# Performance work log

Hardware: AMD Instinct MI355X
Metric: run time of the kernel (lower is better)

Reference implementation:

```python
import jax, jax.numpy as jnp
import numpy as np

N = 60000      # nodes in batch (max_num_cg_nodes_in_batch = 80000)
E = 150000     # edges per edge type
T = 4          # primary edge types (doubled by add_backwards_edges -> 8)
D = 64         # hidden / embedding size
V = 10000      # subtoken vocab
S = 5          # max subtokens per node label
TIMESTEPS = [7, 1]


def setup_inputs() -> dict:
    key = jax.random.key(0)
    ks = jax.random.split(key, 12)
    sc = 1.0 / np.sqrt(D)
    return {
        "node_subtokens": jax.random.randint(ks[0], (N, S), 0, V),
        "adjacency_lists": jax.random.randint(ks[1], (T, E, 2), 0, N),
        "embed_table": jax.random.normal(ks[2], (V, D), jnp.float32) * 0.1,
        "proj_W": jax.random.normal(ks[3], (D, D), jnp.float32) * sc,
        "edge_W0": jax.random.normal(ks[4], (2 * T, D, D), jnp.float32) * sc,
        "edge_W1": jax.random.normal(ks[5], (2 * T, D, D), jnp.float32) * sc,
        "gru0_Wx": jax.random.normal(ks[6], (D, 3 * D), jnp.float32) * sc,
        "gru0_Wh": jax.random.normal(ks[7], (D, 3 * D), jnp.float32) * sc,
        "gru0_b": jnp.zeros((3 * D,), jnp.float32),
        "gru1_Wx": jax.random.normal(ks[8], (2 * D, 3 * D), jnp.float32) * sc,
        "gru1_Wh": jax.random.normal(ks[9], (D, 3 * D), jnp.float32) * sc,
        "gru1_b": jnp.zeros((3 * D,), jnp.float32),
    }


def _gru(x, h, Wx, Wh, b):
    gx = x @ Wx + b          # [N, 3D]
    gh = h @ Wh              # [N, 3D]
    xr, xu, xc = jnp.split(gx, 3, axis=-1)
    hr, hu, hc = jnp.split(gh, 3, axis=-1)
    r = jax.nn.sigmoid(xr + hr)
    u = jax.nn.sigmoid(xu + hu)
    c = jnp.tanh(xc + r * hc)
    return u * h + (1.0 - u) * c


def reference(node_subtokens, adjacency_lists, embed_table, proj_W,
              edge_W0, edge_W1, gru0_Wx, gru0_Wh, gru0_b,
              gru1_Wx, gru1_Wh, gru1_b):
    # Effective edge types: forward + backward (add_backwards_edges=True)
    srcs = jnp.concatenate([adjacency_lists[:, :, 0], adjacency_lists[:, :, 1]], 0)  # [2T, E]
    dsts = jnp.concatenate([adjacency_lists[:, :, 1], adjacency_lists[:, :, 0]], 0)  # [2T, E]
    flat_dsts = dsts.reshape(-1)

    def aggregate(h, edge_W):
        gathered = h[srcs]                                 # [2T, E, D] gather
        msgs = jnp.einsum('ted,tdk->tek', gathered, edge_W)  # per-edge-type transform
        m = jax.ops.segment_max(msgs.reshape(-1, D), flat_dsts, num_segments=N)
        # nodes with no incoming edges get -inf from segment_max -> zero them
        return jnp.where(jnp.isfinite(m), m, 0.0)

    # Subtoken embedding: mean-pool subtoken embeddings, project to hidden
    node_emb = embed_table[node_subtokens].mean(axis=1)    # [N, D]
    h_init = node_emb @ proj_W                             # [N, D]

    # Layer 0: 7 timesteps, no residual
    h = h_init
    for _ in range(TIMESTEPS[0]):
        h = _gru(aggregate(h, edge_W0), h, gru0_Wx, gru0_Wh, gru0_b)

    # Layer 1: 1 timestep, residual from layer index 0 (= initial node states)
    for _ in range(TIMESTEPS[1]):
        msg = aggregate(h, edge_W1)
        h = _gru(jnp.concatenate([h_init, msg], axis=-1), h, gru1_Wx, gru1_Wh, gru1_b)

    return h  # [N, D] final node representations
```

## Files before the change

kernel.cpp:

```cpp
#include <hip/hip_runtime.h>

typedef short v8s __attribute__((ext_vector_type(8)));
typedef float v4f __attribute__((ext_vector_type(4)));

__device__ __forceinline__ unsigned short f2bf(float x) {
  unsigned u = __float_as_uint(x);
  u = u + 0x7FFFu + ((u >> 16) & 1u);
  return (unsigned short)(u >> 16);
}
__device__ __forceinline__ float bf2f(unsigned short b) {
  return __uint_as_float(((unsigned)b) << 16);
}
__device__ __forceinline__ float sigmoidf_(float x) {
  return 1.f / (1.f + __expf(-x));
}
__device__ __forceinline__ float tanhf_(float x) {
  x = fminf(fmaxf(x, -20.f), 20.f);
  float e2 = __expf(2.f * x);
  return (e2 - 1.f) / (e2 + 1.f);
}
__device__ __forceinline__ int swz(int row, int byteInRow) {
  return row * 128 + (byteInRow ^ ((row & 7) << 4));
}

__device__ __forceinline__ void wprep_one(const float* W, unsigned short* O,
                                          int K, int J, int idx) {
  int nkc = K >> 5, nct = J >> 4;
  int j = idx & 7, lane = (idx >> 3) & 63;
  int rest = idx >> 9;
  int ct = rest % nct; rest /= nct;
  int kc = rest % nkc; rest /= nkc;
  int p = rest & 1, t = rest >> 1;
  int row = kc * 32 + (lane >> 4) * 8 + j;
  int col = ct * 16 + (lane & 15);
  float v = W[(size_t)t * K * J + (size_t)row * J + col];
  unsigned short hi = f2bf(v);
  O[idx] = p ? f2bf(v - bf2f(hi)) : hi;
}

__global__ void k_wprep_all(
    const float* eW0, const float* eW1, const float* projW,
    const float* g0Wx, const float* g0Wh, const float* g1Wx, const float* g1Wh,
    unsigned short* eW0f, unsigned short* eW1f, unsigned short* projf,
    unsigned short* g0xf, unsigned short* g0hf,
    unsigned short* g1xf, unsigned short* g1hf) {
  int rel = blockIdx.x * 256 + threadIdx.x;
  if (rel < 65536) { wprep_one(eW0, eW0f, 64, 64, rel); return; }
  rel -= 65536;
  if (rel < 65536) { wprep_one(eW1, eW1f, 64, 64, rel); return; }
  rel -= 65536;
  if (rel < 8192)  { wprep_one(projW, projf, 64, 64, rel); return; }
  rel -= 8192;
  if (rel < 24576) { wprep_one(g0Wx, g0xf, 64, 192, rel); return; }
  rel -= 24576;
  if (rel < 24576) { wprep_one(g0Wh, g0hf, 64, 192, rel); return; }
  rel -= 24576;
  if (rel < 49152) { wprep_one(g1Wx, g1xf, 128, 192, rel); return; }
  rel -= 49152;
  if (rel < 24576) { wprep_one(g1Wh, g1hf, 64, 192, rel); return; }
}

__global__ __launch_bounds__(256) void k_embed(
    const int* __restrict__ toks, const float* __restrict__ embed,
    unsigned short* __restrict__ eh, unsigned short* __restrict__ el, int N) {
  int w = threadIdx.x >> 6, lane = threadIdx.x & 63;
  int n = blockIdx.x * 4 + w;
  if (n >= N) return;
  float acc = 0.f;
#pragma unroll
  for (int s = 0; s < 5; ++s)
    acc += embed[(size_t)toks[n * 5 + s] * 64 + lane];
  float v = acc * 0.2f;
  unsigned short h = f2bf(v);
  eh[(size_t)n * 64 + lane] = h;
  el[(size_t)n * 64 + lane] = f2bf(v - bf2f(h));
}

__global__ void k_counts(const int* __restrict__ adj, int* __restrict__ counts, int E) {
  int e = blockIdx.x * 256 + threadIdx.x;
  if (e >= E) return;
  int t4 = blockIdx.y;
  int2 ab = *(const int2*)&adj[(size_t)(t4 * E + e) * 2];
  atomicAdd(&counts[ab.y], 1);
  atomicAdd(&counts[ab.x], 1);
}

__global__ __launch_bounds__(1024) void k_scan(const int* __restrict__ counts,
                                               int* __restrict__ offsets,
                                               int* __restrict__ cursor, int n) {
  __shared__ int part[1024];
  int tid = threadIdx.x;
  int chunk = (((n + 1023) >> 10) + 3) & ~3;
  int begin = tid * chunk;
  int end = min(begin + chunk, n);
  int s = 0;
  int i = begin;
  for (; i + 4 <= end; i += 4) {
    int4 v = *(const int4*)&counts[i];
    s += v.x + v.y + v.z + v.w;
  }
  for (; i < end; ++i) s += counts[i];
  part[tid] = s;
  __syncthreads();
  for (int off = 1; off < 1024; off <<= 1) {
    int v = (tid >= off) ? part[tid - off] : 0;
    __syncthreads();
    part[tid] += v;
    __syncthreads();
  }
  int run = part[tid] - s;
  i = begin;
  for (; i + 4 <= end; i += 4) {
    int4 c = *(const int4*)&counts[i];
    int4 o;
    o.x = run; o.y = run + c.x; o.z = o.y + c.y; o.w = o.z + c.z;
    *(int4*)&offsets[i] = o;
    *(int4*)&cursor[i] = o;
    run = o.w + c.w;
  }
  for (; i < end; ++i) {
    offsets[i] = run; cursor[i] = run; run += counts[i];
  }
  if (tid == 1023) offsets[n] = part[1023];
}

__global__ void k_fill(const int* __restrict__ adj, int* __restrict__ cursor,
                       int* __restrict__ entries, int E, int N) {
  int e = blockIdx.x * 256 + threadIdx.x;
  if (e >= E) return;
  int t4 = blockIdx.y;
  int2 ab = *(const int2*)&adj[(size_t)(t4 * E + e) * 2];
  int p1 = atomicAdd(&cursor[ab.y], 1);
  entries[p1] = t4 * N + ab.x;
  int p2 = atomicAdd(&cursor[ab.x], 1);
  entries[p2] = (t4 + 4) * N + ab.y;
}

__global__ __launch_bounds__(256) void k_proj(
    const unsigned short* __restrict__ A0h, const unsigned short* __restrict__ A0l,
    const unsigned short* __restrict__ Wf,
    unsigned short* __restrict__ h_hi, unsigned short* __restrict__ h_lo,
    unsigned short* __restrict__ hinit_b, int N) {
  int tid = threadIdx.x;
  int wv = tid >> 6, lane = tid & 63;
  int lr = lane & 15, lg = lane >> 4;
  int m0 = blockIdx.x * 128 + wv * 32;
  v4f acc[2][4] = {};
#pragma unroll
  for (int kc = 0; kc < 2; ++kc) {
    v8s ah[2], al[2];
#pragma unroll
    for (int mt = 0; mt < 2; ++mt) {
      int row = min(m0 + mt * 16 + lr, N - 1);
      size_t off = (size_t)row * 64 + kc * 32 + lg * 8;
      ah[mt] = *(const v8s*)&A0h[off];
      al[mt] = *(const v8s*)&A0l[off];
    }
#pragma unroll
    for (int ct = 0; ct < 4; ++ct) {
      v8s bh = *(const v8s*)&Wf[((size_t)(kc * 4 + ct)) * 512 + lane * 8];
      v8s bl = *(const v8s*)&Wf[((size_t)((2 + kc) * 4 + ct)) * 512 + lane * 8];
#pragma unroll
      for (int mt = 0; mt < 2; ++mt) {
        acc[mt][ct] = __builtin_amdgcn_mfma_f32_16x16x32_bf16(ah[mt], bh, acc[mt][ct], 0, 0, 0);
        acc[mt][ct] = __builtin_amdgcn_mfma_f32_16x16x32_bf16(al[mt], bh, acc[mt][ct], 0, 0, 0);
        acc[mt][ct] = __builtin_amdgcn_mfma_f32_16x16x32_bf16(ah[mt], bl, acc[mt][ct], 0, 0, 0);
      }
    }
  }
#pragma unroll
  for (int ct = 0; ct < 4; ++ct)
#pragma unroll
    for (int mt = 0; mt < 2; ++mt)
#pragma unroll
      for (int r = 0; r < 4; ++r) {
        int m = m0 + mt * 16 + lg * 4 + r;
        if (m >= N) continue;
        int col = ct * 16 + lr;
        float v = acc[mt][ct][r];
        unsigned short hb = f2bf(v);
        h_hi[(size_t)m * 64 + col] = hb;
        h_lo[(size_t)m * 64 + col] = f2bf(v - bf2f(hb));
        hinit_b[(size_t)m * 64 + col] = hb;
      }
}

__global__ __launch_bounds__(256) void k_mm_t(
    const unsigned short* __restrict__ A0h, const unsigned short* __restrict__ A0l,
    const unsigned short* __restrict__ Wf, unsigned short* __restrict__ C16,
    int N) {
  int tid = threadIdx.x;
  int wv = tid >> 6, lane = tid & 63;
  int lr = lane & 15, lg = lane >> 4;
  int y = blockIdx.y;
  const unsigned short* W0 = Wf + (size_t)y * 8192;
  const unsigned short* W1 = Wf + (size_t)(y + 4) * 8192;
  unsigned short* C0 = C16 + (size_t)y * N * 64;
  unsigned short* C1 = C16 + (size_t)(y + 4) * N * 64;
  int m0 = blockIdx.x * 128 + wv * 32;
  v4f acc0[2][4] = {}, acc1[2][4] = {};
#pragma unroll
  for (int kc = 0; kc < 2; ++kc) {
    v8s ah[2], al[2];
#pragma unroll
    for (int mt = 0; mt < 2; ++mt) {
      int row = min(m0 + mt * 16 + lr, N - 1);
      size_t off = (size_t)row * 64 + kc * 32 + lg * 8;
      ah[mt] = *(const v8s*)&A0h[off];
      al[mt] = *(const v8s*)&A0l[off];
    }
#pragma unroll
    for (int ct = 0; ct < 4; ++ct) {
      v8s bh0 = *(const v8s*)&W0[((size_t)(kc * 4 + ct)) * 512 + lane * 8];
      v8s bl0 = *(const v8s*)&W0[((size_t)((2 + kc) * 4 + ct)) * 512 + lane * 8];
      v8s bh1 = *(const v8s*)&W1[((size_t)(kc * 4 + ct)) * 512 + lane * 8];
      v8s bl1 = *(const v8s*)&W1[((size_t)((2 + kc) * 4 + ct)) * 512 + lane * 8];
#pragma unroll
      for (int mt = 0; mt < 2; ++mt) {
        acc0[mt][ct] = __builtin_amdgcn_mfma_f32_16x16x32_bf16(ah[mt], bh0, acc0[mt][ct], 0, 0, 0);
        acc0[mt][ct] = __builtin_amdgcn_mfma_f32_16x16x32_bf16(al[mt], bh0, acc0[mt][ct], 0, 0, 0);
        acc0[mt][ct] = __builtin_amdgcn_mfma_f32_16x16x32_bf16(ah[mt], bl0, acc0[mt][ct], 0, 0, 0);
        acc1[mt][ct] = __builtin_amdgcn_mfma_f32_16x16x32_bf16(ah[mt], bh1, acc1[mt][ct], 0, 0, 0);
        acc1[mt][ct] = __builtin_amdgcn_mfma_f32_16x16x32_bf16(al[mt], bh1, acc1[mt][ct], 0, 0, 0);
        acc1[mt][ct] = __builtin_amdgcn_mfma_f32_16x16x32_bf16(ah[mt], bl1, acc1[mt][ct], 0, 0, 0);
      }
    }
  }
#pragma unroll
  for (int ct = 0; ct < 4; ++ct)
#pragma unroll
    for (int mt = 0; mt < 2; ++mt)
#pragma unroll
      for (int r = 0; r < 4; ++r) {
        int m = m0 + mt * 16 + lg * 4 + r;
        if (m < N) {
          C0[(size_t)m * 64 + ct * 16 + lr] = f2bf(acc0[mt][ct][r]);
          C1[(size_t)m * 64 + ct * 16 + lr] = f2bf(acc1[mt][ct][r]);
        }
      }
}

__global__ __launch_bounds__(256) void k_aggmax(
    const unsigned short* __restrict__ Htb, const int* __restrict__ offsets,
    const int* __restrict__ entries, unsigned short* __restrict__ mh, int N) {
  int w = threadIdx.x >> 6, lane = threadIdx.x & 63;
  int n = blockIdx.x * 4 + w;
  if (n >= N) return;
  int beg = offsets[n], end = offsets[n + 1];
  int g = lane >> 4, q = lane & 15;
  float a0 = -3.4e38f, a1 = a0, a2 = a0, a3 = a0;
  float b0 = a0, b1 = a0, b2 = a0, b3 = a0;
  float c0 = a0, c1 = a0, c2 = a0, c3 = a0;
  float d0 = a0, d1 = a0, d2 = a0, d3 = a0;
  int i = beg;
  for (; i + 16 <= end; i += 16) {
    int eA = entries[i + g];
    int eB = entries[i + 4 + g];
    int eC = entries[i + 8 + g];
    int eD = entries[i + 12 + g];
    ushort4 va = *(const ushort4*)&Htb[(size_t)eA * 64 + q * 4];
    ushort4 vb = *(const ushort4*)&Htb[(size_t)eB * 64 + q * 4];
    ushort4 vc = *(const ushort4*)&Htb[(size_t)eC * 64 + q * 4];
    ushort4 vd = *(const ushort4*)&Htb[(size_t)eD * 64 + q * 4];
    a0 = fmaxf(a0, bf2f(va.x)); a1 = fmaxf(a1, bf2f(va.y));
    a2 = fmaxf(a2, bf2f(va.z)); a3 = fmaxf(a3, bf2f(va.w));
    b0 = fmaxf(b0, bf2f(vb.x)); b1 = fmaxf(b1, bf2f(vb.y));
    b2 = fmaxf(b2, bf2f(vb.z)); b3 = fmaxf(b3, bf2f(vb.w));
    c0 = fmaxf(c0, bf2f(vc.x)); c1 = fmaxf(c1, bf2f(vc.y));
    c2 = fmaxf(c2, bf2f(vc.z)); c3 = fmaxf(c3, bf2f(vc.w));
    d0 = fmaxf(d0, bf2f(vd.x)); d1 = fmaxf(d1, bf2f(vd.y));
    d2 = fmaxf(d2, bf2f(vd.z)); d3 = fmaxf(d3, bf2f(vd.w));
  }
  for (; i + 8 <= end; i += 8) {
    int eA = entries[i + g];
    int eB = entries[i + 4 + g];
    ushort4 va = *(const ushort4*)&Htb[(size_t)eA * 64 + q * 4];
    ushort4 vb = *(const ushort4*)&Htb[(size_t)eB * 64 + q * 4];
    a0 = fmaxf(a0, bf2f(va.x)); a1 = fmaxf(a1, bf2f(va.y));
    a2 = fmaxf(a2, bf2f(va.z)); a3 = fmaxf(a3, bf2f(va.w));
    b0 = fmaxf(b0, bf2f(vb.x)); b1 = fmaxf(b1, bf2f(vb.y));
    b2 = fmaxf(b2, bf2f(vb.z)); b3 = fmaxf(b3, bf2f(vb.w));
  }
  for (; i < end; i += 4) {
    int idx = min(i + g, end - 1);
    int e = entries[idx];
    ushort4 va = *(const ushort4*)&Htb[(size_t)e * 64 + q * 4];
    a0 = fmaxf(a0, bf2f(va.x)); a1 = fmaxf(a1, bf2f(va.y));
    a2 = fmaxf(a2, bf2f(va.z)); a3 = fmaxf(a3, bf2f(va.w));
  }
  a0 = fmaxf(fmaxf(a0, b0), fmaxf(c0, d0));
  a1 = fmaxf(fmaxf(a1, b1), fmaxf(c1, d1));
  a2 = fmaxf(fmaxf(a2, b2), fmaxf(c2, d2));
  a3 = fmaxf(fmaxf(a3, b3), fmaxf(c3, d3));
  a0 = fmaxf(a0, __shfl_xor(a0, 16)); a1 = fmaxf(a1, __shfl_xor(a1, 16));
  a2 = fmaxf(a2, __shfl_xor(a2, 16)); a3 = fmaxf(a3, __shfl_xor(a3, 16));
  a0 = fmaxf(a0, __shfl_xor(a0, 32)); a1 = fmaxf(a1, __shfl_xor(a1, 32));
  a2 = fmaxf(a2, __shfl_xor(a2, 32)); a3 = fmaxf(a3, __shfl_xor(a3, 32));
  if (g == 0) {
    ushort4 o;
    if (end > beg) {
      o.x = f2bf(a0); o.y = f2bf(a1); o.z = f2bf(a2); o.w = f2bf(a3);
    } else {
      o.x = 0; o.y = 0; o.z = 0; o.w = 0;
    }
    *(ushort4*)&mh[(size_t)n * 64 + q * 4] = o;
  }
}

template <int FINAL>
__global__ __launch_bounds__(256) void k_gt(
    const unsigned short* __restrict__ x0, const unsigned short* __restrict__ x1,
    unsigned short* __restrict__ hh, unsigned short* __restrict__ hl,
    const unsigned short* __restrict__ Wxf, const unsigned short* __restrict__ Whf,
    const float* __restrict__ bias, const unsigned short* __restrict__ eWf,
    unsigned short* __restrict__ HtW, float* __restrict__ outF, int N) {
  __shared__ __align__(16) char lds_hs[FINAL ? 16 : 128 * 128];
  int tid = threadIdx.x;
  int wv = tid >> 6, lane = tid & 63;
  int lr = lane & 15, lg = lane >> 4;
  int lbase = wv * 32;
  int m0 = blockIdx.x * 128 + lbase;

  const int NKCX = FINAL ? 4 : 2;
  v4f acc[2][12] = {};
  v4f acch[2][4] = {};
#pragma unroll
  for (int kc = 0; kc < NKCX; ++kc) {
    const unsigned short* X = (FINAL && kc >= 2) ? x1 : x0;
    int kcl = kc & 1;
    v8s ax[2];
#pragma unroll
    for (int mt = 0; mt < 2; ++mt) {
      int row = min(m0 + mt * 16 + lr, N - 1);
      ax[mt] = *(const v8s*)&X[(size_t)row * 64 + kcl * 32 + lg * 8];
    }
#pragma unroll
    for (int ct = 0; ct < 12; ++ct) {
      v8s bh = *(const v8s*)&Wxf[((size_t)(kc * 12 + ct)) * 512 + lane * 8];
      v8s bl = *(const v8s*)&Wxf[((size_t)((NKCX + kc) * 12 + ct)) * 512 + lane * 8];
#pragma unroll
      for (int mt = 0; mt < 2; ++mt) {
        acc[mt][ct] = __builtin_amdgcn_mfma_f32_16x16x32_bf16(ax[mt], bh, acc[mt][ct], 0, 0, 0);
        acc[mt][ct] = __builtin_amdgcn_mfma_f32_16x16x32_bf16(ax[mt], bl, acc[mt][ct], 0, 0, 0);
      }
    }
  }
#pragma unroll
  for (int kc = 0; kc < 2; ++kc) {
    v8s ah[2], al[2];
#pragma unroll
    for (int mt = 0; mt < 2; ++mt) {
      int row = min(m0 + mt * 16 + lr, N - 1);
      size_t off = (size_t)row * 64 + kc * 32 + lg * 8;
      ah[mt] = *(const v8s*)&hh[off];
      al[mt] = *(const v8s*)&hl[off];
    }
#pragma unroll
    for (int ct = 0; ct < 12; ++ct) {
      v8s bh = *(const v8s*)&Whf[((size_t)(kc * 12 + ct)) * 512 + lane * 8];
      v8s bl = *(const v8s*)&Whf[((size_t)((2 + kc) * 12 + ct)) * 512 + lane * 8];
#pragma unroll
      for (int mt = 0; mt < 2; ++mt) {
        v4f* d = (ct < 8) ? &acc[mt][ct] : &acch[mt][ct - 8];
        *d = __builtin_amdgcn_mfma_f32_16x16x32_bf16(ah[mt], bh, *d, 0, 0, 0);
        *d = __builtin_amdgcn_mfma_f32_16x16x32_bf16(al[mt], bh, *d, 0, 0, 0);
        *d = __builtin_amdgcn_mfma_f32_16x16x32_bf16(ah[mt], bl, *d, 0, 0, 0);
      }
    }
  }
#pragma unroll
  for (int mt = 0; mt < 2; ++mt)
#pragma unroll
    for (int ctg = 0; ctg < 4; ++ctg)
#pragma unroll
      for (int r = 0; r < 4; ++r) {
        int m = m0 + mt * 16 + lg * 4 + r;
        int col = ctg * 16 + lr;
        unsigned short hbv = hh[(size_t)min(m, N - 1) * 64 + col];
        unsigned short hlv = hl[(size_t)min(m, N - 1) * 64 + col];
        float hv = bf2f(hbv) + bf2f(hlv);
        float rr = sigmoidf_(acc[mt][ctg][r] + bias[col]);
        float uu = sigmoidf_(acc[mt][ctg + 4][r] + bias[64 + col]);
        float cc = tanhf_(acc[mt][ctg + 8][r] + bias[128 + col] + rr * acch[mt][ctg][r]);
        float ho = uu * hv + (1.f - uu) * cc;
        if (FINAL) {
          if (m < N) outF[(size_t)m * 64 + col] = ho;
        } else {
          unsigned short ohi = f2bf(ho);
          unsigned short olo = f2bf(ho - bf2f(ohi));
          if (m < N) {
            hh[(size_t)m * 64 + col] = ohi;
            hl[(size_t)m * 64 + col] = olo;
          }
          int row = lbase + mt * 16 + lg * 4 + r;
          *(unsigned short*)(lds_hs + swz(row, col * 2)) = ohi;
        }
      }

  if (FINAL) return;

  v8s tah[2][2];
#pragma unroll
  for (int kc = 0; kc < 2; ++kc)
#pragma unroll
    for (int mt = 0; mt < 2; ++mt) {
      int row = lbase + mt * 16 + lr;
      tah[kc][mt] = *(const v8s*)(lds_hs + swz(row, kc * 64 + lg * 16));
    }
#pragma unroll
  for (int y = 0; y < 4; ++y) {
    const unsigned short* W0 = eWf + (size_t)y * 8192;
    const unsigned short* W1 = eWf + (size_t)(y + 4) * 8192;
    unsigned short* C0 = HtW + (size_t)y * N * 64;
    unsigned short* C1 = HtW + (size_t)(y + 4) * N * 64;
    v4f acc0[2][4] = {}, acc1[2][4] = {};
#pragma unroll
    for (int kc = 0; kc < 2; ++kc)
#pragma unroll
      for (int ct = 0; ct < 4; ++ct) {
        v8s bh0 = *(const v8s*)&W0[((size_t)(kc * 4 + ct)) * 512 + lane * 8];
        v8s bl0 = *(const v8s*)&W0[((size_t)((2 + kc) * 4 + ct)) * 512 + lane * 8];
        v8s bh1 = *(const v8s*)&W1[((size_t)(kc * 4 + ct)) * 512 + lane * 8];
        v8s bl1 = *(const v8s*)&W1[((size_t)((2 + kc) * 4 + ct)) * 512 + lane * 8];
#pragma unroll
        for (int mt = 0; mt < 2; ++mt) {
          acc0[mt][ct] = __builtin_amdgcn_mfma_f32_16x16x32_bf16(tah[kc][mt], bh0, acc0[mt][ct], 0, 0, 0);
          acc0[mt][ct] = __builtin_amdgcn_mfma_f32_16x16x32_bf16(tah[kc][mt], bl0, acc0[mt][ct], 0, 0, 0);
          acc1[mt][ct] = __builtin_amdgcn_mfma_f32_16x16x32_bf16(tah[kc][mt], bh1, acc1[mt][ct], 0, 0, 0);
          acc1[mt][ct] = __builtin_amdgcn_mfma_f32_16x16x32_bf16(tah[kc][mt], bl1, acc1[mt][ct], 0, 0, 0);
        }
      }
#pragma unroll
    for (int ct = 0; ct < 4; ++ct)
#pragma unroll
      for (int mt = 0; mt < 2; ++mt)
#pragma unroll
        for (int r = 0; r < 4; ++r) {
          int m = m0 + mt * 16 + lg * 4 + r;
          if (m < N) {
            C0[(size_t)m * 64 + ct * 16 + lr] = f2bf(acc0[mt][ct][r]);
            C1[(size_t)m * 64 + ct * 16 + lr] = f2bf(acc1[mt][ct][r]);
          }
        }
  }
}

extern "C" void kernel_launch(void* const* d_in, const int* in_sizes, int n_in,
                              void* d_out, int out_size, void* d_ws, size_t ws_size,
                              hipStream_t stream) {
  const int*   toks  = (const int*)d_in[0];
  const int*   adj   = (const int*)d_in[1];
  const float* embed = (const float*)d_in[2];
  const float* projW = (const float*)d_in[3];
  const float* eW0   = (const float*)d_in[4];
  const float* eW1   = (const float*)d_in[5];
  const float* g0Wx  = (const float*)d_in[6];
  const float* g0Wh  = (const float*)d_in[7];
  const float* g0b   = (const float*)d_in[8];
  const float* g1Wx  = (const float*)d_in[9];
  const float* g1Wh  = (const float*)d_in[10];
  const float* g1b   = (const float*)d_in[11];
  float* out = (float*)d_out;

  int N = in_sizes[0] / 5;
  int E = in_sizes[1] / 8;
  size_t ND = (size_t)N * 64;

  char* p = (char*)d_ws;
  unsigned short* Htb     = (unsigned short*)p; p += 8 * ND * 2;
  unsigned short* h_hi    = (unsigned short*)p; p += ND * 2;
  unsigned short* h_lo    = (unsigned short*)p; p += ND * 2;
  unsigned short* hinit_b = (unsigned short*)p; p += ND * 2;
  unsigned short* m_hi    = (unsigned short*)p; p += ND * 2;
  int* offsets = (int*)p; p += (size_t)(N + 64) * sizeof(int);
  int* cnt_cur = (int*)p; p += (size_t)(N + 64) * sizeof(int);
  int* entries = (int*)p; p += (size_t)8 * E * sizeof(int);
  unsigned short* eW0f  = (unsigned short*)p; p += 65536 * 2;
  unsigned short* eW1f  = (unsigned short*)p; p += 65536 * 2;
  unsigned short* projf = (unsigned short*)p; p += 8192 * 2;
  unsigned short* g0xf  = (unsigned short*)p; p += 24576 * 2;
  unsigned short* g0hf  = (unsigned short*)p; p += 24576 * 2;
  unsigned short* g1xf  = (unsigned short*)p; p += 49152 * 2;
  unsigned short* g1hf  = (unsigned short*)p; p += 24576 * 2;
  if ((size_t)(p - (char*)d_ws) > ws_size) return;

  unsigned short* emb_h = Htb;
  unsigned short* emb_l = Htb + ND;

  int g128 = (N + 127) / 128;
  int g4 = (N + 3) / 4;

  k_wprep_all<<<1024, 256, 0, stream>>>(eW0, eW1, projW, g0Wx, g0Wh, g1Wx, g1Wh,
                                        eW0f, eW1f, projf, g0xf, g0hf, g1xf, g1hf);
  hipMemsetAsync(cnt_cur, 0, (size_t)N * sizeof(int), stream);
  dim3 egrid((E + 255) / 256, 4);
  k_counts<<<egrid, 256, 0, stream>>>(adj, cnt_cur, E);
  k_embed<<<g4, 256, 0, stream>>>(toks, embed, emb_h, emb_l, N);
  k_proj<<<g128, 256, 0, stream>>>(emb_h, emb_l, projf, h_hi, h_lo, hinit_b, N);
  k_scan<<<1, 1024, 0, stream>>>(cnt_cur, offsets, cnt_cur, N);
  k_fill<<<egrid, 256, 0, stream>>>(adj, cnt_cur, entries, E, N);
  k_mm_t<<<dim3(g128, 4), 256, 0, stream>>>(h_hi, h_lo, eW0f, Htb, N);

  for (int it = 0; it < 7; ++it) {
    k_aggmax<<<g4, 256, 0, stream>>>(Htb, offsets, entries, m_hi, N);
    const unsigned short* ef = (it < 6) ? eW0f : eW1f;
    k_gt<0><<<g128, 256, 0, stream>>>(m_hi, nullptr, h_hi, h_lo,
                                      g0xf, g0hf, g0b, ef, Htb, nullptr, N);
  }
  k_aggmax<<<g4, 256, 0, stream>>>(Htb, offsets, entries, m_hi, N);
  k_gt<1><<<g128, 256, 0, stream>>>(hinit_b, m_hi, h_hi, h_lo,
                                    g1xf, g1hf, g1b, nullptr, nullptr, out, N);
}
```

Measured before the change: 1.089 ms.

## Merge setup kernels into two launches and shuffle-broadcast edge indices in aggmax

The separate count, embed and weight-prep kernels become one block-partitioned launch, and the fill and projection kernels become a second, cutting the setup from six kernel launches to two plus the scan. In the max-aggregation kernel, each 16-edge chunk now loads its indices once per lane and broadcasts them with shuffles. This replaces the 16/8/4 remainder loops with a single clamped loop. The clamping re-reads the last edge for partial chunks, which does redundant gather work for nodes with few edges but gives uniform control flow.

```diff
diff --git a/kernel.cpp b/kernel.cpp
--- a/kernel.cpp
+++ b/kernel.cpp
@@ -38,13 +38,43 @@
   O[idx] = p ? f2bf(v - bf2f(hi)) : hi;
 }
 
-__global__ void k_wprep_all(
+__global__ __launch_bounds__(256) void k_setup1(
+    const int* __restrict__ adj, int* __restrict__ counts, int E, int ex,
+    const int* __restrict__ toks, const float* __restrict__ embed,
+    unsigned short* __restrict__ eh, unsigned short* __restrict__ el, int N, int g4,
     const float* eW0, const float* eW1, const float* projW,
     const float* g0Wx, const float* g0Wh, const float* g1Wx, const float* g1Wh,
     unsigned short* eW0f, unsigned short* eW1f, unsigned short* projf,
     unsigned short* g0xf, unsigned short* g0hf,
     unsigned short* g1xf, unsigned short* g1hf) {
-  int rel = blockIdx.x * 256 + threadIdx.x;
+  int b = blockIdx.x;
+  int tid = threadIdx.x;
+  if (b < 4 * ex) {
+    int t4 = b / ex, eb = b % ex;
+    int e = eb * 256 + tid;
+    if (e >= E) return;
+    int2 ab = *(const int2*)&adj[(size_t)(t4 * E + e) * 2];
+    atomicAdd(&counts[ab.y], 1);
+    atomicAdd(&counts[ab.x], 1);
+    return;
+  }
+  b -= 4 * ex;
+  if (b < g4) {
+    int w = tid >> 6, lane = tid & 63;
+    int n = b * 4 + w;
+    if (n >= N) return;
+    float acc = 0.f;
+#pragma unroll
+    for (int s = 0; s < 5; ++s)
+      acc += embed[(size_t)toks[n * 5 + s] * 64 + lane];
+    float v = acc * 0.2f;
+    unsigned short h = f2bf(v);
+    eh[(size_t)n * 64 + lane] = h;
+    el[(size_t)n * 64 + lane] = f2bf(v - bf2f(h));
+    return;
+  }
+  b -= g4;
+  int rel = b * 256 + tid;
   if (rel < 65536) { wprep_one(eW0, eW0f, 64, 64, rel); return; }
   rel -= 65536;
   if (rel < 65536) { wprep_one(eW1, eW1f, 64, 64, rel); return; }
@@ -60,31 +90,6 @@
   if (rel < 24576) { wprep_one(g1Wh, g1hf, 64, 192, rel); return; }
 }
 
-__global__ __launch_bounds__(256) void k_embed(
-    const int* __restrict__ toks, const float* __restrict__ embed,
-    unsigned short* __restrict__ eh, unsigned short* __restrict__ el, int N) {
-  int w = threadIdx.x >> 6, lane = threadIdx.x & 63;
-  int n = blockIdx.x * 4 + w;
-  if (n >= N) return;
-  float acc = 0.f;
-#pragma unroll
-  for (int s = 0; s < 5; ++s)
-    acc += embed[(size_t)toks[n * 5 + s] * 64 + lane];
-  float v = acc * 0.2f;
-  unsigned short h = f2bf(v);
-  eh[(size_t)n * 64 + lane] = h;
-  el[(size_t)n * 64 + lane] = f2bf(v - bf2f(h));
-}
-
-__global__ void k_counts(const int* __restrict__ adj, int* __restrict__ counts, int E) {
-  int e = blockIdx.x * 256 + threadIdx.x;
-  if (e >= E) return;
-  int t4 = blockIdx.y;
-  int2 ab = *(const int2*)&adj[(size_t)(t4 * E + e) * 2];
-  atomicAdd(&counts[ab.y], 1);
-  atomicAdd(&counts[ab.x], 1);
-}
-
 __global__ __launch_bounds__(1024) void k_scan(const int* __restrict__ counts,
                                                int* __restrict__ offsets,
                                                int* __restrict__ cursor, int n) {
@@ -124,27 +129,30 @@
   if (tid == 1023) offsets[n] = part[1023];
 }
 
-__global__ void k_fill(const int* __restrict__ adj, int* __restrict__ cursor,
-                       int* __restrict__ entries, int E, int N) {
-  int e = blockIdx.x * 256 + threadIdx.x;
-  if (e >= E) return;
-  int t4 = blockIdx.y;
-  int2 ab = *(const int2*)&adj[(size_t)(t4 * E + e) * 2];
-  int p1 = atomicAdd(&cursor[ab.y], 1);
-  entries[p1] = t4 * N + ab.x;
-  int p2 = atomicAdd(&cursor[ab.x], 1);
-  entries[p2] = (t4 + 4) * N + ab.y;
-}
-
-__global__ __launch_bounds__(256) void k_proj(
+__global__ __launch_bounds__(256) void k_setup2(
+    const int* __restrict__ adj, int* __restrict__ cursor,
+    int* __restrict__ entries, int E, int ex, int N,
     const unsigned short* __restrict__ A0h, const unsigned short* __restrict__ A0l,
     const unsigned short* __restrict__ Wf,
     unsigned short* __restrict__ h_hi, unsigned short* __restrict__ h_lo,
-    unsigned short* __restrict__ hinit_b, int N) {
+    unsigned short* __restrict__ hinit_b) {
+  int b = blockIdx.x;
   int tid = threadIdx.x;
+  if (b < 4 * ex) {
+    int t4 = b / ex, eb = b % ex;
+    int e = eb * 256 + tid;
+    if (e >= E) return;
+    int2 ab = *(const int2*)&adj[(size_t)(t4 * E + e) * 2];
+    int p1 = atomicAdd(&cursor[ab.y], 1);
+    entries[p1] = t4 * N + ab.x;
+    int p2 = atomicAdd(&cursor[ab.x], 1);
+    entries[p2] = (t4 + 4) * N + ab.y;
+    return;
+  }
+  b -= 4 * ex;
   int wv = tid >> 6, lane = tid & 63;
   int lr = lane & 15, lg = lane >> 4;
-  int m0 = blockIdx.x * 128 + wv * 32;
+  int m0 = b * 128 + wv * 32;
   v4f acc[2][4] = {};
 #pragma unroll
   for (int kc = 0; kc < 2; ++kc) {
@@ -252,12 +260,13 @@
   float b0 = a0, b1 = a0, b2 = a0, b3 = a0;
   float c0 = a0, c1 = a0, c2 = a0, c3 = a0;
   float d0 = a0, d1 = a0, d2 = a0, d3 = a0;
-  int i = beg;
-  for (; i + 16 <= end; i += 16) {
-    int eA = entries[i + g];
-    int eB = entries[i + 4 + g];
-    int eC = entries[i + 8 + g];
-    int eD = entries[i + 12 + g];
+  for (int i = beg; i < end; i += 16) {
+    int li = min(i + (lane & 15), end - 1);
+    int ei = entries[li];
+    int eA = __shfl(ei, g);
+    int eB = __shfl(ei, g + 4);
+    int eC = __shfl(ei, g + 8);
+    int eD = __shfl(ei, g + 12);
     ushort4 va = *(const ushort4*)&Htb[(size_t)eA * 64 + q * 4];
     ushort4 vb = *(const ushort4*)&Htb[(size_t)eB * 64 + q * 4];
     ushort4 vc = *(const ushort4*)&Htb[(size_t)eC * 64 + q * 4];
@@ -270,23 +279,6 @@
     c2 = fmaxf(c2, bf2f(vc.z)); c3 = fmaxf(c3, bf2f(vc.w));
     d0 = fmaxf(d0, bf2f(vd.x)); d1 = fmaxf(d1, bf2f(vd.y));
     d2 = fmaxf(d2, bf2f(vd.z)); d3 = fmaxf(d3, bf2f(vd.w));
-  }
-  for (; i + 8 <= end; i += 8) {
-    int eA = entries[i + g];
-    int eB = entries[i + 4 + g];
-    ushort4 va = *(const ushort4*)&Htb[(size_t)eA * 64 + q * 4];
-    ushort4 vb = *(const ushort4*)&Htb[(size_t)eB * 64 + q * 4];
-    a0 = fmaxf(a0, bf2f(va.x)); a1 = fmaxf(a1, bf2f(va.y));
-    a2 = fmaxf(a2, bf2f(va.z)); a3 = fmaxf(a3, bf2f(va.w));
-    b0 = fmaxf(b0, bf2f(vb.x)); b1 = fmaxf(b1, bf2f(vb.y));
-    b2 = fmaxf(b2, bf2f(vb.z)); b3 = fmaxf(b3, bf2f(vb.w));
-  }
-  for (; i < end; i += 4) {
-    int idx = min(i + g, end - 1);
-    int e = entries[idx];
-    ushort4 va = *(const ushort4*)&Htb[(size_t)e * 64 + q * 4];
-    a0 = fmaxf(a0, bf2f(va.x)); a1 = fmaxf(a1, bf2f(va.y));
-    a2 = fmaxf(a2, bf2f(va.z)); a3 = fmaxf(a3, bf2f(va.w));
   }
   a0 = fmaxf(fmaxf(a0, b0), fmaxf(c0, d0));
   a1 = fmaxf(fmaxf(a1, b1), fmaxf(c1, d1));
@@ -489,16 +481,17 @@
 
   int g128 = (N + 127) / 128;
   int g4 = (N + 3) / 4;
-
-  k_wprep_all<<<1024, 256, 0, stream>>>(eW0, eW1, projW, g0Wx, g0Wh, g1Wx, g1Wh,
-                                        eW0f, eW1f, projf, g0xf, g0hf, g1xf, g1hf);
+  int ex = (E + 255) / 256;
+
   hipMemsetAsync(cnt_cur, 0, (size_t)N * sizeof(int), stream);
-  dim3 egrid((E + 255) / 256, 4);
-  k_counts<<<egrid, 256, 0, stream>>>(adj, cnt_cur, E);
-  k_embed<<<g4, 256, 0, stream>>>(toks, embed, emb_h, emb_l, N);
-  k_proj<<<g128, 256, 0, stream>>>(emb_h, emb_l, projf, h_hi, h_lo, hinit_b, N);
+  k_setup1<<<4 * ex + g4 + 1024, 256, 0, stream>>>(
+      adj, cnt_cur, E, ex, toks, embed, emb_h, emb_l, N, g4,
+      eW0, eW1, projW, g0Wx, g0Wh, g1Wx, g1Wh,
+      eW0f, eW1f, projf, g0xf, g0hf, g1xf, g1hf);
   k_scan<<<1, 1024, 0, stream>>>(cnt_cur, offsets, cnt_cur, N);
-  k_fill<<<egrid, 256, 0, stream>>>(adj, cnt_cur, entries, E, N);
+  k_setup2<<<4 * ex + g128, 256, 0, stream>>>(
+      adj, cnt_cur, entries, E, ex, N,
+      emb_h, emb_l, projf, h_hi, h_lo, hinit_b);
   k_mm_t<<<dim3(g128, 4), 256, 0, stream>>>(h_hi, h_lo, eW0f, Htb, N);
 
   for (int it = 0; it < 7; ++it) {
```

Result: no change. 1.089 ms (-0.0%).
